# Kernel optimization log

Measured on AMD Instinct MI355X. Metric: run time of the kernel, lower is better.

Reference implementation:

```python
import jax, jax.numpy as jnp
import numpy as np

B, T, IN, CELL, OUT = 512, 32, 512, 128, 128


def setup_inputs() -> dict:
    key = jax.random.key(0)
    ks = jax.random.split(key, 6)
    d = IN + CELL
    w = lambda k, shape, fan: jax.random.normal(k, shape, jnp.float32) / np.sqrt(fan).astype(np.float32)
    return {
        "x": jax.random.normal(ks[0], (B, T, IN), jnp.float32),
        "Wf": w(ks[1], (d, CELL), d), "bf": jnp.zeros((CELL,), jnp.float32),
        "Wi1": w(ks[2], (d, CELL), d), "bi1": jnp.zeros((CELL,), jnp.float32),
        "Wi2": w(ks[3], (d, CELL), d), "bi2": jnp.zeros((CELL,), jnp.float32),
        "Wo": w(ks[4], (d, CELL), d), "bo": jnp.zeros((CELL,), jnp.float32),
        "Wc": w(ks[5], (CELL, OUT), CELL), "bc": jnp.zeros((OUT,), jnp.float32),
    }


def reference(x, Wf, bf, Wi1, bi1, Wi2, bi2, Wo, bo, Wc, bc):
    # Faithful to MyLSTM.forward: loop runs x.shape[1] times; each iteration
    # concatenates the FULL [B,T,CELL] cell_state with the FULL [B,T,IN] x
    # (x is never sliced per step). Only the last iteration's output matters,
    # but we carry it through the scan to match the loop structure exactly.
    Tn = x.shape[1]
    c0 = jnp.zeros(x.shape[:2] + (Wf.shape[1],), x.dtype)
    out0 = jnp.zeros(x.shape[:2] + (Wc.shape[1],), x.dtype)

    def step(carry, _):
        c, _prev_out = carry
        inp = jnp.concatenate([c, x], axis=-1)  # [B,T,CELL+IN]
        f = jax.nn.sigmoid(inp @ Wf + bf)
        c = c * f + jax.nn.sigmoid(inp @ Wi1 + bi1) * jnp.tanh(inp @ Wi2 + bi2)
        o = jax.nn.sigmoid(inp @ Wo + bo) * jnp.tanh(c)
        out = jax.nn.softmax(o @ Wc + bc, axis=2)  # out_features != 1 branch
        return (c, out), None

    (c, out), _ = jax.lax.scan(step, (c0, out0), None, length=Tn)
    return out, c
```

## Files before the change

### kernel.cpp

```cpp
#include <hip/hip_runtime.h>
#include <stdint.h>

#define ROWS  16384
#define CELL  128
#define INF   512
#define RPB   16
#define NSTEP 32

typedef _Float16 f16x8 __attribute__((ext_vector_type(8)));
typedef _Float16 f16x4 __attribute__((ext_vector_type(4)));
typedef float    f32x4 __attribute__((ext_vector_type(4)));

#define MFMA16(a, b, c) __builtin_amdgcn_mfma_f32_16x16x32_f16((a), (b), (c), 0, 0, 0)

#define AOFF  0
#define XOFF  65536
#define WCOFF 327680
#define WSTOT 344064

__device__ __forceinline__ unsigned short f2h_bits(float f) {
  _Float16 h = (_Float16)f;
  return *(unsigned short*)&h;
}
__device__ __forceinline__ float sig_f(float z) {
  return __builtin_amdgcn_rcpf(1.f + __expf(-z));
}
__device__ __forceinline__ float tanh_f(float z) {
  return 1.f - 2.f * __builtin_amdgcn_rcpf(__expf(2.f * z) + 1.f);
}

__global__ __launch_bounds__(256) void prep_kernel(
    const float* __restrict__ Wf, const float* __restrict__ Wi1,
    const float* __restrict__ Wi2, const float* __restrict__ Wo,
    const float* __restrict__ Wc, unsigned short* __restrict__ ws) {
  int id = blockIdx.x * blockDim.x + threadIdx.x;
  if (id >= WSTOT) return;
  const float* Wg[4] = {Wf, Wi1, Wi2, Wo};
  float v;
  int k, n, base;
  if (id < XOFF) {
    int g = id >> 14, r = id & 16383;
    k = r >> 7; n = r & 127;
    v = Wg[g][k * CELL + n];
    base = g * 16384;
  } else if (id < WCOFF) {
    int t = id - XOFF;
    int g = t >> 16, r = t & 65535;
    k = r >> 7; n = r & 127;
    v = Wg[g][(CELL + k) * CELL + n];
    base = XOFF + g * 65536;
  } else {
    int r = id - WCOFF;
    k = r >> 7; n = r & 127;
    v = Wc[k * CELL + n];
    base = WCOFF;
  }
  int ks = k >> 5, kk = k & 31;
  int lane = ((kk >> 3) << 4) | (n & 15);
  int j = kk & 7, nb = n >> 4;
  ws[base + ((ks * 8 + nb) * 64 + lane) * 8 + j] = f2h_bits(v);
}

__global__ __launch_bounds__(512, 4) void lstm_kernel(
    const float* __restrict__ x,
    const float* __restrict__ bf_, const float* __restrict__ bi1,
    const float* __restrict__ bi2, const float* __restrict__ bo,
    const float* __restrict__ bc,
    const unsigned short* __restrict__ ws, float* __restrict__ out) {

  __shared__ _Float16 cF[2][16][136];
  __shared__ union {
    _Float16 xs[16][520];
    struct {
      float    s[16][132];
      _Float16 o[16][136];
    } ep;
  } uS;

  const int tid  = threadIdx.x;
  const int lane = tid & 63;
  const int w    = tid >> 6;
  const int n16  = lane & 15;
  const int g4   = lane >> 4;
  const int col  = w * 16 + n16;
  const int r0   = blockIdx.x * RPB;

  const _Float16* Aw  = (const _Float16*)ws + AOFF;
  const _Float16* Xw  = (const _Float16*)ws + XOFF;
  const _Float16* Wcw = (const _Float16*)ws + WCOFF;

  {
    const float* xb = x + (size_t)r0 * INF;
#pragma unroll
    for (int i = 0; i < 4; ++i) {
      int flat = tid + i * 512;
      int row = flat >> 7, c4 = flat & 127;
      const float4 v = ((const float4*)(xb + (size_t)row * INF))[c4];
      f16x4 h = {(_Float16)v.x, (_Float16)v.y, (_Float16)v.z, (_Float16)v.w};
      *(f16x4*)&uS.xs[row][c4 * 4] = h;
    }
  }
  __syncthreads();

  f32x4 u[4];
#pragma unroll
  for (int g = 0; g < 4; ++g)
#pragma unroll
    for (int i = 0; i < 4; ++i) u[g][i] = 0.f;

#pragma unroll 4
  for (int ks = 0; ks < 16; ++ks) {
    f16x8 a = *(const f16x8*)&uS.xs[n16][ks * 32 + g4 * 8];
#pragma unroll
    for (int g = 0; g < 4; ++g) {
      f16x8 b = *(const f16x8*)(Xw + g * 65536 + ((ks * 8 + w) * 64 + lane) * 8);
      u[g] = MFMA16(a, b, u[g]);
    }
  }
  {
    float b0 = bf_[col], b1 = bi1[col], b2 = bi2[col], b3 = bo[col];
#pragma unroll
    for (int i = 0; i < 4; ++i) {
      u[0][i] += b0; u[1][i] += b1; u[2][i] += b2; u[3][i] += b3;
    }
  }

  f16x8 wr[3][4];
#pragma unroll
  for (int g = 0; g < 3; ++g)
#pragma unroll
    for (int ks = 0; ks < 4; ++ks)
      wr[g][ks] = *(const f16x8*)(Aw + g * 16384 + ((ks * 8 + w) * 64 + lane) * 8);

  f32x4 cr;
#pragma unroll
  for (int i = 0; i < 4; ++i) {
    float c0 = sig_f(u[1][i]) * tanh_f(u[2][i]);
    cr[i] = c0;
    cF[0][g4 * 4 + i][col] = (_Float16)c0;
  }
  __syncthreads();

#pragma unroll 1
  for (int t = 1; t < NSTEP - 1; ++t) {
    const int rb = (t + 1) & 1, wb = t & 1;
    f16x8 a[4];
#pragma unroll
    for (int ks = 0; ks < 4; ++ks)
      a[ks] = *(const f16x8*)&cF[rb][n16][ks * 32 + g4 * 8];
    f32x4 zf = u[0], zi1 = u[1], zi2 = u[2];
#pragma unroll
    for (int ks = 0; ks < 4; ++ks) {
      zf  = MFMA16(a[ks], wr[0][ks], zf);
      zi1 = MFMA16(a[ks], wr[1][ks], zi1);
      zi2 = MFMA16(a[ks], wr[2][ks], zi2);
    }
#pragma unroll
    for (int i = 0; i < 4; ++i) {
      float fg = sig_f(zf[i]);
      float ig = sig_f(zi1[i]);
      float gg = tanh_f(zi2[i]);
      float cn = fmaf(cr[i], fg, ig * gg);
      cr[i] = cn;
      cF[wb][g4 * 4 + i][col] = (_Float16)cn;
    }
    __syncthreads();
  }

  {
    f16x8 a[4];
#pragma unroll
    for (int ks = 0; ks < 4; ++ks)
      a[ks] = *(const f16x8*)&cF[0][n16][ks * 32 + g4 * 8];
    f32x4 zf = u[0], zi1 = u[1], zi2 = u[2], zo = u[3];
#pragma unroll
    for (int ks = 0; ks < 4; ++ks) {
      f16x8 bo_frag = *(const f16x8*)(Aw + 3 * 16384 + ((ks * 8 + w) * 64 + lane) * 8);
      zf  = MFMA16(a[ks], wr[0][ks], zf);
      zi1 = MFMA16(a[ks], wr[1][ks], zi1);
      zi2 = MFMA16(a[ks], wr[2][ks], zi2);
      zo  = MFMA16(a[ks], bo_frag, zo);
    }
#pragma unroll
    for (int i = 0; i < 4; ++i) {
      float fg = sig_f(zf[i]);
      float ig = sig_f(zi1[i]);
      float gg = tanh_f(zi2[i]);
      float cn = fmaf(cr[i], fg, ig * gg);
      cr[i] = cn;
      float ov = sig_f(zo[i]) * tanh_f(cn);
      uS.ep.o[g4 * 4 + i][col] = (_Float16)ov;
    }
    __syncthreads();
  }

  {
    f32x4 sacc;
#pragma unroll
    for (int i = 0; i < 4; ++i) sacc[i] = 0.f;
#pragma unroll
    for (int ks = 0; ks < 4; ++ks) {
      f16x8 a = *(const f16x8*)&uS.ep.o[n16][ks * 32 + g4 * 8];
      f16x8 b = *(const f16x8*)(Wcw + ((ks * 8 + w) * 64 + lane) * 8);
      sacc = MFMA16(a, b, sacc);
    }
    float bv = bc[col];
#pragma unroll
    for (int i = 0; i < 4; ++i)
      uS.ep.s[g4 * 4 + i][col] = sacc[i] + bv;
    __syncthreads();

#pragma unroll
    for (int rr = 0; rr < 2; ++rr) {
      int r = w * 2 + rr;
      float v0 = uS.ep.s[r][lane];
      float v1 = uS.ep.s[r][lane + 64];
      float m = fmaxf(v0, v1);
#pragma unroll
      for (int off = 32; off; off >>= 1) m = fmaxf(m, __shfl_xor(m, off, 64));
      float e0 = __expf(v0 - m), e1 = __expf(v1 - m);
      float sm = e0 + e1;
#pragma unroll
      for (int off = 32; off; off >>= 1) sm += __shfl_xor(sm, off, 64);
      float inv = __builtin_amdgcn_rcpf(sm);
      size_t base = (size_t)(r0 + r) * 128;
      out[base + lane]      = e0 * inv;
      out[base + lane + 64] = e1 * inv;
    }

#pragma unroll
    for (int i = 0; i < 4; ++i)
      out[(size_t)ROWS * 128 + (size_t)(r0 + g4 * 4 + i) * 128 + col] = cr[i];
  }
}

extern "C" void kernel_launch(void* const* d_in, const int* in_sizes, int n_in,
                              void* d_out, int out_size, void* d_ws, size_t ws_size,
                              hipStream_t stream) {
  const float* x   = (const float*)d_in[0];
  const float* Wf  = (const float*)d_in[1];
  const float* bf_ = (const float*)d_in[2];
  const float* Wi1 = (const float*)d_in[3];
  const float* bi1 = (const float*)d_in[4];
  const float* Wi2 = (const float*)d_in[5];
  const float* bi2 = (const float*)d_in[6];
  const float* Wo  = (const float*)d_in[7];
  const float* bo  = (const float*)d_in[8];
  const float* Wc  = (const float*)d_in[9];
  const float* bc  = (const float*)d_in[10];
  unsigned short* ws = (unsigned short*)d_ws;
  float* out = (float*)d_out;

  hipLaunchKernelGGL(prep_kernel, dim3((WSTOT + 255) / 256), dim3(256), 0, stream,
                     Wf, Wi1, Wi2, Wo, Wc, ws);
  hipLaunchKernelGGL(lstm_kernel, dim3(ROWS / RPB), dim3(512), 0, stream,
                     x, bf_, bi1, bi2, bo, bc, ws, out);
}
```

Before: 170.3 us.

## Prescale gate weights by log2e and transpose MFMA operands for vectorized stores

```diff
diff --git a/kernel.cpp b/kernel.cpp
--- a/kernel.cpp
+++ b/kernel.cpp
@@ -18,15 +18,18 @@
 #define WCOFF 327680
 #define WSTOT 344064
 
+#define LOG2E  1.44269504f
+#define LOG2E2 2.88539008f
+
 __device__ __forceinline__ unsigned short f2h_bits(float f) {
   _Float16 h = (_Float16)f;
   return *(unsigned short*)&h;
 }
-__device__ __forceinline__ float sig_f(float z) {
-  return __builtin_amdgcn_rcpf(1.f + __expf(-z));
-}
-__device__ __forceinline__ float tanh_f(float z) {
-  return 1.f - 2.f * __builtin_amdgcn_rcpf(__expf(2.f * z) + 1.f);
+__device__ __forceinline__ float sig2(float z) {
+  return __builtin_amdgcn_rcpf(1.f + __builtin_amdgcn_exp2f(-z));
+}
+__device__ __forceinline__ float tanh2(float z) {
+  return 1.f - 2.f * __builtin_amdgcn_rcpf(__builtin_amdgcn_exp2f(z) + 1.f);
 }
 
 __global__ __launch_bounds__(256) void prep_kernel(
@@ -36,18 +39,19 @@
   int id = blockIdx.x * blockDim.x + threadIdx.x;
   if (id >= WSTOT) return;
   const float* Wg[4] = {Wf, Wi1, Wi2, Wo};
+  const float scl[4] = {LOG2E, LOG2E, LOG2E2, LOG2E};
   float v;
   int k, n, base;
   if (id < XOFF) {
     int g = id >> 14, r = id & 16383;
     k = r >> 7; n = r & 127;
-    v = Wg[g][k * CELL + n];
+    v = Wg[g][k * CELL + n] * scl[g];
     base = g * 16384;
   } else if (id < WCOFF) {
     int t = id - XOFF;
     int g = t >> 16, r = t & 65535;
     k = r >> 7; n = r & 127;
-    v = Wg[g][(CELL + k) * CELL + n];
+    v = Wg[g][(CELL + k) * CELL + n] * scl[g];
     base = XOFF + g * 65536;
   } else {
     int r = id - WCOFF;
@@ -82,7 +86,7 @@
   const int w    = tid >> 6;
   const int n16  = lane & 15;
   const int g4   = lane >> 4;
-  const int col  = w * 16 + n16;
+  const int col0 = w * 16 + g4 * 4;
   const int r0   = blockIdx.x * RPB;
 
   const _Float16* Aw  = (const _Float16*)ws + AOFF;
@@ -114,14 +118,20 @@
 #pragma unroll
     for (int g = 0; g < 4; ++g) {
       f16x8 b = *(const f16x8*)(Xw + g * 65536 + ((ks * 8 + w) * 64 + lane) * 8);
-      u[g] = MFMA16(a, b, u[g]);
-    }
-  }
-  {
-    float b0 = bf_[col], b1 = bi1[col], b2 = bi2[col], b3 = bo[col];
-#pragma unroll
-    for (int i = 0; i < 4; ++i) {
-      u[0][i] += b0; u[1][i] += b1; u[2][i] += b2; u[3][i] += b3;
+      u[g] = MFMA16(b, a, u[g]);
+    }
+  }
+  {
+    f32x4 b0 = *(const f32x4*)&bf_[col0];
+    f32x4 b1 = *(const f32x4*)&bi1[col0];
+    f32x4 b2 = *(const f32x4*)&bi2[col0];
+    f32x4 b3 = *(const f32x4*)&bo[col0];
+#pragma unroll
+    for (int i = 0; i < 4; ++i) {
+      u[0][i] = fmaf(b0[i], LOG2E,  u[0][i]);
+      u[1][i] = fmaf(b1[i], LOG2E,  u[1][i]);
+      u[2][i] = fmaf(b2[i], LOG2E2, u[2][i]);
+      u[3][i] = fmaf(b3[i], LOG2E,  u[3][i]);
     }
   }
 
@@ -133,11 +143,15 @@
       wr[g][ks] = *(const f16x8*)(Aw + g * 16384 + ((ks * 8 + w) * 64 + lane) * 8);
 
   f32x4 cr;
-#pragma unroll
-  for (int i = 0; i < 4; ++i) {
-    float c0 = sig_f(u[1][i]) * tanh_f(u[2][i]);
-    cr[i] = c0;
-    cF[0][g4 * 4 + i][col] = (_Float16)c0;
+  {
+    f16x4 hv;
+#pragma unroll
+    for (int i = 0; i < 4; ++i) {
+      float c0 = sig2(u[1][i]) * tanh2(u[2][i]);
+      cr[i] = c0;
+      hv[i] = (_Float16)c0;
+    }
+    *(f16x4*)&cF[0][n16][col0] = hv;
   }
   __syncthreads();
 
@@ -151,19 +165,21 @@
     f32x4 zf = u[0], zi1 = u[1], zi2 = u[2];
 #pragma unroll
     for (int ks = 0; ks < 4; ++ks) {
-      zf  = MFMA16(a[ks], wr[0][ks], zf);
-      zi1 = MFMA16(a[ks], wr[1][ks], zi1);
-      zi2 = MFMA16(a[ks], wr[2][ks], zi2);
-    }
-#pragma unroll
-    for (int i = 0; i < 4; ++i) {
-      float fg = sig_f(zf[i]);
-      float ig = sig_f(zi1[i]);
-      float gg = tanh_f(zi2[i]);
+      zf  = MFMA16(wr[0][ks], a[ks], zf);
+      zi1 = MFMA16(wr[1][ks], a[ks], zi1);
+      zi2 = MFMA16(wr[2][ks], a[ks], zi2);
+    }
+    f16x4 hv;
+#pragma unroll
+    for (int i = 0; i < 4; ++i) {
+      float fg = sig2(zf[i]);
+      float ig = sig2(zi1[i]);
+      float gg = tanh2(zi2[i]);
       float cn = fmaf(cr[i], fg, ig * gg);
       cr[i] = cn;
-      cF[wb][g4 * 4 + i][col] = (_Float16)cn;
-    }
+      hv[i] = (_Float16)cn;
+    }
+    *(f16x4*)&cF[wb][n16][col0] = hv;
     __syncthreads();
   }
 
@@ -176,21 +192,24 @@
 #pragma unroll
     for (int ks = 0; ks < 4; ++ks) {
       f16x8 bo_frag = *(const f16x8*)(Aw + 3 * 16384 + ((ks * 8 + w) * 64 + lane) * 8);
-      zf  = MFMA16(a[ks], wr[0][ks], zf);
-      zi1 = MFMA16(a[ks], wr[1][ks], zi1);
-      zi2 = MFMA16(a[ks], wr[2][ks], zi2);
-      zo  = MFMA16(a[ks], bo_frag, zo);
-    }
-#pragma unroll
-    for (int i = 0; i < 4; ++i) {
-      float fg = sig_f(zf[i]);
-      float ig = sig_f(zi1[i]);
-      float gg = tanh_f(zi2[i]);
+      zf  = MFMA16(wr[0][ks], a[ks], zf);
+      zi1 = MFMA16(wr[1][ks], a[ks], zi1);
+      zi2 = MFMA16(wr[2][ks], a[ks], zi2);
+      zo  = MFMA16(bo_frag,  a[ks], zo);
+    }
+    f16x4 hv;
+#pragma unroll
+    for (int i = 0; i < 4; ++i) {
+      float fg = sig2(zf[i]);
+      float ig = sig2(zi1[i]);
+      float gg = tanh2(zi2[i]);
       float cn = fmaf(cr[i], fg, ig * gg);
       cr[i] = cn;
-      float ov = sig_f(zo[i]) * tanh_f(cn);
-      uS.ep.o[g4 * 4 + i][col] = (_Float16)ov;
-    }
+      float ov = sig2(zo[i]) * tanh2(cn * LOG2E2);
+      hv[i] = (_Float16)ov;
+    }
+    __syncthreads();
+    *(f16x4*)&uS.ep.o[n16][col0] = hv;
     __syncthreads();
   }
 
@@ -202,12 +221,12 @@
     for (int ks = 0; ks < 4; ++ks) {
       f16x8 a = *(const f16x8*)&uS.ep.o[n16][ks * 32 + g4 * 8];
       f16x8 b = *(const f16x8*)(Wcw + ((ks * 8 + w) * 64 + lane) * 8);
-      sacc = MFMA16(a, b, sacc);
-    }
-    float bv = bc[col];
-#pragma unroll
-    for (int i = 0; i < 4; ++i)
-      uS.ep.s[g4 * 4 + i][col] = sacc[i] + bv;
+      sacc = MFMA16(b, a, sacc);
+    }
+    f32x4 bcv = *(const f32x4*)&bc[col0];
+#pragma unroll
+    for (int i = 0; i < 4; ++i) sacc[i] += bcv[i];
+    *(f32x4*)&uS.ep.s[n16][col0] = sacc;
     __syncthreads();
 
 #pragma unroll
@@ -228,9 +247,7 @@
       out[base + lane + 64] = e1 * inv;
     }
 
-#pragma unroll
-    for (int i = 0; i < 4; ++i)
-      out[(size_t)ROWS * 128 + (size_t)(r0 + g4 * 4 + i) * 128 + col] = cr[i];
+    *(f32x4*)&out[(size_t)ROWS * 128 + (size_t)(r0 + n16) * 128 + col0] = cr;
   }
 }
 
```

After: 168.5 us. Within noise of the previous version (-1.1%).
